# Kernel optimization log

Hardware: AMD Instinct MI355X
Metric: run time of the kernel (lower is better)

The kernel has to match this reference:

```python
import jax, jax.numpy as jnp
import numpy as np

N_NODES = 50000
N_EDGES = 800000
D = 128
SAME_W = 0.3
CROSS_W = 1.0


def setup_inputs() -> dict:
    key = jax.random.key(0)
    k1, k2, k3, k4, k5 = jax.random.split(key, 5)
    x = jax.random.normal(k1, (N_NODES, D), dtype=jnp.float32)
    edge_index = jax.random.randint(k2, (2, N_EDGES), 0, N_NODES, dtype=jnp.int64)
    edge_weight = jax.random.uniform(k3, (N_EDGES,), dtype=jnp.float32)
    Wr1 = jax.random.normal(k4, (D, D), dtype=jnp.float32) * (1.0 / np.sqrt(D))
    Wr2 = jax.random.normal(k5, (D, D), dtype=jnp.float32) * (1.0 / np.sqrt(D))
    return {"x": x, "edge_index": edge_index, "edge_weight": edge_weight,
            "Wr1": Wr1, "Wr2": Wr2, "cell_len": 20000}


def _node_types(idx, cell_len):
    # get_node_types: type 0 if idx <= cell_len, else 1 (note the <=, faithful to source)
    return (idx > cell_len).astype(jnp.int32)


def _conv_layer(x, src, dst, per_edge_w, Wr, n_nodes):
    # gather -> weight -> scatter-mean -> + root linear
    msg = x[src] * per_edge_w[:, None]                       # [E, D]
    agg = jax.ops.segment_sum(msg, dst, num_segments=n_nodes)  # [N, D]
    cnt = jax.ops.segment_sum(jnp.ones_like(per_edge_w), dst, num_segments=n_nodes)
    agg = agg / jnp.maximum(cnt, 1.0)[:, None]               # mean aggr (0 if no edges)
    return agg + x @ Wr.T                                     # lin_r, bias=False


def reference(x, edge_index, edge_weight, Wr1, Wr2, cell_len):
    src, dst = edge_index[0], edge_index[1]
    same = _node_types(src, cell_len) == _node_types(dst, cell_len)
    type_w = jnp.where(same, SAME_W, CROSS_W).astype(x.dtype)
    w = type_w * edge_weight                                  # [E]
    n_nodes = x.shape[0]
    h = _conv_layer(x, src, dst, w, Wr1, n_nodes)
    out = _conv_layer(h, src, dst, w, Wr2, n_nodes)
    return out
```

## Files before the change

kernel.cpp:

```cpp
#include <hip/hip_runtime.h>
#include <cstdint>
#include <cstddef>

#define D 128
#define SAME_W 0.3f
#define CROSS_W 1.0f
#define NSLICE 8
#define CAP 64
#define P1_EPT 8
#define SLAB 131072
#define GEMM_BLOCKS 512

using bf16x8 = __attribute__((ext_vector_type(8))) __bf16;
using f32x4  = __attribute__((ext_vector_type(4))) float;

__device__ __forceinline__ unsigned bf16rne(float f) {
    unsigned u = __float_as_uint(f);
    return (u + 0x7FFFu + ((u >> 16) & 1u)) >> 16;
}

__global__ __launch_bounds__(256) void k_pre(
    const int* __restrict__ src, const int* __restrict__ dst,
    const float* __restrict__ ew, const int* __restrict__ cell_len,
    int* __restrict__ scnt, uint2* __restrict__ ebuf, int E, int sliceLen,
    int nFillC,
    const float4* __restrict__ x4, uint2* __restrict__ xh2,
    uint2* __restrict__ xl2, unsigned* __restrict__ xq, int nvec, int nSplit,
    const float* __restrict__ W1, const float* __restrict__ W2,
    unsigned* __restrict__ wsh, unsigned* __restrict__ w12h,
    unsigned* __restrict__ w12l)
{
    const int b = blockIdx.x;
    if (b < nFillC) {
        __shared__ int lcnt[NSLICE];
        __shared__ int lbase[NSLICE];
        const int t = threadIdx.x;
        if (t < NSLICE) lcnt[t] = 0;
        __syncthreads();
        const int c = *cell_len;
        const int base = b * (256 * P1_EPT) + t;
        int   sl[P1_EPT], rk[P1_EPT];
        uint2 en[P1_EPT];
        #pragma unroll
        for (int u = 0; u < P1_EPT; ++u) {
            int e = base + u * 256;
            sl[u] = -1;
            if (e < E) {
                int d = __builtin_nontemporal_load(&dst[e]);
                int s = __builtin_nontemporal_load(&src[e]);
                float w = __builtin_nontemporal_load(&ew[e]);
                float wt = w * (((s > c) == (d > c)) ? SAME_W : CROSS_W);
                int slice = d / sliceLen;
                sl[u] = slice;
                en[u].x = (unsigned)d | ((unsigned)s << 16);
                en[u].y = bf16rne(wt);
                rk[u] = atomicAdd(&lcnt[slice], 1);
            }
        }
        __syncthreads();
        if (t < NSLICE) lbase[t] = atomicAdd(&scnt[t], lcnt[t]);
        __syncthreads();
        #pragma unroll
        for (int u = 0; u < P1_EPT; ++u) {
            if (sl[u] >= 0) {
                int idx = lbase[sl[u]] + rk[u];
                if (idx < SLAB)
                    ebuf[(size_t)sl[u] * SLAB + idx] = en[u];
            }
        }
    } else if (b < nFillC + nSplit) {
        int i = (b - nFillC) * 256 + threadIdx.x;
        if (i >= nvec) return;
        float4 v = x4[i];
        unsigned h0 = bf16rne(v.x), h1 = bf16rne(v.y),
                 h2 = bf16rne(v.z), h3 = bf16rne(v.w);
        xh2[i] = make_uint2(h0 | (h1 << 16), h2 | (h3 << 16));
        float r0 = v.x - __uint_as_float(h0 << 16);
        float r1 = v.y - __uint_as_float(h1 << 16);
        float r2 = v.z - __uint_as_float(h2 << 16);
        float r3 = v.w - __uint_as_float(h3 << 16);
        xl2[i] = make_uint2(bf16rne(r0) | (bf16rne(r1) << 16),
                            bf16rne(r2) | (bf16rne(r3) << 16));
        int q = __builtin_amdgcn_cvt_pk_fp8_f32(v.x, v.y, 0, false);
        q = __builtin_amdgcn_cvt_pk_fp8_f32(v.z, v.w, q, true);
        xq[i] = (unsigned)q;
    } else {
        int t = (b - nFillC - nSplit) * 256 + threadIdx.x;
        int j = t >> 6, kp = t & 63;
        int k0 = kp * 2;
        float d0 = 0.f, d1 = 0.f;
        #pragma unroll 4
        for (int m = 0; m < D; ++m) {
            float a = W2[j * D + m];
            d0 = fmaf(a, W1[m * D + k0], d0);
            d1 = fmaf(a, W1[m * D + k0 + 1], d1);
        }
        float s0 = W1[j * D + k0] + W2[j * D + k0];
        float s1 = W1[j * D + k0 + 1] + W2[j * D + k0 + 1];
        wsh[j * 64 + kp] = bf16rne(s0) | (bf16rne(s1) << 16);
        unsigned h0 = bf16rne(d0), h1 = bf16rne(d1);
        w12h[j * 64 + kp] = h0 | (h1 << 16);
        float r0 = d0 - __uint_as_float(h0 << 16);
        float r1 = d1 - __uint_as_float(h1 << 16);
        w12l[j * 64 + kp] = bf16rne(r0) | (bf16rne(r1) << 16);
    }
}

__global__ __launch_bounds__(256) void k_scatter(const uint2* __restrict__ ebuf,
                                                 const int* __restrict__ scnt,
                                                 int* __restrict__ cnt,
                                                 unsigned* __restrict__ meta) {
    const int s = blockIdx.x & (NSLICE - 1);
    const int chunk = blockIdx.x >> 3;
    const int n = min(scnt[s], SLAB);
    const uint2* buf = ebuf + (size_t)s * SLAB;
    const int step = (GEMM_BLOCKS / NSLICE) * 256;
    for (int i = chunk * 256 + threadIdx.x; i < n; i += step) {
        uint2 en = buf[i];
        int d = en.x & 0xFFFFu;
        unsigned mw = (en.x >> 16) | (en.y << 16);
        int pos = atomicAdd(&cnt[d], 1);
        if (pos < CAP) meta[d * CAP + pos] = mw;
    }
}

template <bool EMIT_FP8>
__global__ __launch_bounds__(256) void k_agg_fp8(const unsigned short* __restrict__ xq,
                                                 const uint4* __restrict__ meta4,
                                                 const int* __restrict__ cnt,
                                                 unsigned* __restrict__ outb,
                                                 unsigned short* __restrict__ outq,
                                                 int N) {
    int gid = blockIdx.x * blockDim.x + threadIdx.x;
    int node = gid >> 6;
    int lane = gid & 63;
    if (node >= N) return;
    const int cn0 = cnt[node];
    const int cn = min(cn0, CAP);
    const uint4* mrow = meta4 + (size_t)node * (CAP / 4);
    float ax0 = 0.f, ay0 = 0.f, ax1 = 0.f, ay1 = 0.f;
    int i = 0;
    #pragma unroll 1
    for (; i + 16 <= cn; i += 16) {
        uint4 mq[4];
        #pragma unroll
        for (int u = 0; u < 4; ++u) mq[u] = mrow[(i >> 2) + u];
        unsigned short v[16];
        #pragma unroll
        for (int u = 0; u < 16; ++u) {
            unsigned m = ((const unsigned*)mq)[u];
            v[u] = xq[(size_t)(m & 0xFFFFu) * 64 + lane];
        }
        #pragma unroll
        for (int u = 0; u < 16; ++u) {
            unsigned m = ((const unsigned*)mq)[u];
            float wt = __uint_as_float(m & 0xFFFF0000u);
            float vx = __builtin_amdgcn_cvt_f32_fp8((unsigned)v[u], 0);
            float vy = __builtin_amdgcn_cvt_f32_fp8((unsigned)v[u], 1);
            if (u & 1) { ax1 = fmaf(vx, wt, ax1); ay1 = fmaf(vy, wt, ay1); }
            else       { ax0 = fmaf(vx, wt, ax0); ay0 = fmaf(vy, wt, ay0); }
        }
    }
    #pragma unroll 1
    for (; i + 4 <= cn; i += 4) {
        uint4 mq = mrow[i >> 2];
        unsigned short v[4];
        #pragma unroll
        for (int u = 0; u < 4; ++u)
            v[u] = xq[(size_t)(((const unsigned*)&mq)[u] & 0xFFFFu) * 64 + lane];
        #pragma unroll
        for (int u = 0; u < 4; ++u) {
            unsigned m = ((const unsigned*)&mq)[u];
            float wt = __uint_as_float(m & 0xFFFF0000u);
            float vx = __builtin_amdgcn_cvt_f32_fp8((unsigned)v[u], 0);
            float vy = __builtin_amdgcn_cvt_f32_fp8((unsigned)v[u], 1);
            if (u & 1) { ax1 = fmaf(vx, wt, ax1); ay1 = fmaf(vy, wt, ay1); }
            else       { ax0 = fmaf(vx, wt, ax0); ay0 = fmaf(vy, wt, ay0); }
        }
    }
    for (; i < cn; ++i) {
        unsigned m = ((const unsigned*)mrow)[i];
        float wt = __uint_as_float(m & 0xFFFF0000u);
        unsigned short v = xq[(size_t)(m & 0xFFFFu) * 64 + lane];
        ax0 = fmaf(__builtin_amdgcn_cvt_f32_fp8((unsigned)v, 0), wt, ax0);
        ay0 = fmaf(__builtin_amdgcn_cvt_f32_fp8((unsigned)v, 1), wt, ay0);
    }
    const float scale = 1.0f / (float)max(cn0, 1);
    const float rx = (ax0 + ax1) * scale, ry = (ay0 + ay1) * scale;
    outb[(size_t)node * 64 + lane] = bf16rne(rx) | (bf16rne(ry) << 16);
    if (EMIT_FP8) {
        int q = __builtin_amdgcn_cvt_pk_fp8_f32(rx, ry, 0, false);
        outq[(size_t)node * 64 + lane] = (unsigned short)(q & 0xFFFF);
    }
}

__global__ __launch_bounds__(256, 2) void k_gemm2(
    const uint4* __restrict__ xh4, const uint4* __restrict__ xl4,
    const uint4* __restrict__ a1h4,
    const uint4* __restrict__ w12h4, const uint4* __restrict__ w12l4,
    const uint4* __restrict__ wsh4,
    const unsigned* __restrict__ a2b,
    float* __restrict__ fout, int N, int nTiles)
{
    const int t = threadIdx.x;
    const int wave = t >> 6, lane = t & 63;
    const int j0 = wave * 32;
    const int lr = lane & 15;
    const int q  = lane >> 4;

    union FU { uint4 u; bf16x8 v; };

    FU wA[2][4], wB[2][4], wC[2][4];
    #pragma unroll
    for (int jt = 0; jt < 2; ++jt) {
        const int brow = (j0 + jt * 16 + lr) * 16 + q;
        #pragma unroll
        for (int ks = 0; ks < 4; ++ks) {
            wA[jt][ks].u = w12h4[brow + ks * 4];
            wB[jt][ks].u = w12l4[brow + ks * 4];
            wC[jt][ks].u = wsh4[brow + ks * 4];
        }
    }

#define LOAD_TILE(BX, BL, BA, BC, TILE) do {                                   \
    int row_ = (TILE) * 16 + lr; if (row_ > N - 1) row_ = N - 1;               \
    const int ar_ = row_ * 16 + q;                                             \
    _Pragma("unroll")                                                          \
    for (int ks = 0; ks < 4; ++ks) {                                           \
        BX[ks].u = xh4[ar_ + ks * 4];                                          \
        BL[ks].u = xl4[ar_ + ks * 4];                                          \
        BA[ks].u = a1h4[ar_ + ks * 4];                                         \
    }                                                                          \
    _Pragma("unroll")                                                          \
    for (int jt = 0; jt < 2; ++jt)                                             \
        _Pragma("unroll")                                                      \
        for (int r = 0; r < 4; ++r) {                                          \
            int rr_ = (TILE) * 16 + q * 4 + r; if (rr_ > N - 1) rr_ = N - 1;   \
            BC[jt * 4 + r] = a2b[(size_t)rr_ * 64 + ((j0 + jt * 16 + lr) >> 1)]; \
        }                                                                      \
} while (0)

#define COMPUTE_STORE(BX, BL, BA, BC, TILE) do {                               \
    f32x4 c_[2];                                                               \
    c_[0] = (f32x4){0.f, 0.f, 0.f, 0.f};                                       \
    c_[1] = (f32x4){0.f, 0.f, 0.f, 0.f};                                       \
    _Pragma("unroll")                                                          \
    for (int jt = 0; jt < 2; ++jt)                                             \
        _Pragma("unroll")                                                      \
        for (int ks = 0; ks < 4; ++ks) {                                       \
            c_[jt] = __builtin_amdgcn_mfma_f32_16x16x32_bf16(BX[ks].v, wA[jt][ks].v, c_[jt], 0, 0, 0); \
            c_[jt] = __builtin_amdgcn_mfma_f32_16x16x32_bf16(BL[ks].v, wA[jt][ks].v, c_[jt], 0, 0, 0); \
            c_[jt] = __builtin_amdgcn_mfma_f32_16x16x32_bf16(BX[ks].v, wB[jt][ks].v, c_[jt], 0, 0, 0); \
            c_[jt] = __builtin_amdgcn_mfma_f32_16x16x32_bf16(BA[ks].v, wC[jt][ks].v, c_[jt], 0, 0, 0); \
        }                                                                      \
    _Pragma("unroll")                                                          \
    for (int jt = 0; jt < 2; ++jt)                                             \
        _Pragma("unroll")                                                      \
        for (int r = 0; r < 4; ++r) {                                          \
            int rr_ = (TILE) * 16 + q * 4 + r;                                 \
            if (rr_ < N) {                                                     \
                unsigned w_ = BC[jt * 4 + r];                                  \
                float ci_ = __uint_as_float((lr & 1) ? (w_ & 0xFFFF0000u) : (w_ << 16)); \
                fout[(size_t)rr_ * D + j0 + jt * 16 + lr] = c_[jt][r] + ci_;   \
            }                                                                  \
        }                                                                      \
} while (0)

    FU Axh[4], Axl[4], Aa1[4]; unsigned Aci[8];
    FU Bxh[4], Bxl[4], Ba1[4]; unsigned Bci[8];

    int tile = blockIdx.x;
    const int step = gridDim.x;
    if (tile >= nTiles) return;
    LOAD_TILE(Axh, Axl, Aa1, Aci, tile);
    while (true) {
        int tn = tile + step;
        if (tn < nTiles) LOAD_TILE(Bxh, Bxl, Ba1, Bci, tn);
        COMPUTE_STORE(Axh, Axl, Aa1, Aci, tile);
        tile = tn;
        if (tile >= nTiles) break;
        tn = tile + step;
        if (tn < nTiles) LOAD_TILE(Axh, Axl, Aa1, Aci, tn);
        COMPUTE_STORE(Bxh, Bxl, Ba1, Bci, tile);
        tile = tn;
        if (tile >= nTiles) break;
    }
#undef LOAD_TILE
#undef COMPUTE_STORE
}

extern "C" void kernel_launch(void* const* d_in, const int* in_sizes, int n_in,
                              void* d_out, int out_size, void* d_ws, size_t ws_size,
                              hipStream_t stream) {
    const float* x        = (const float*)d_in[0];
    const int*   ei       = (const int*)d_in[1];
    const float* ew       = (const float*)d_in[2];
    const float* Wr1      = (const float*)d_in[3];
    const float* Wr2      = (const float*)d_in[4];
    const int*   cell_len = (const int*)d_in[5];

    const int N = in_sizes[0] / D;
    const int E = in_sizes[1] / 2;
    const int* src = ei;
    const int* dst = ei + E;

    char* ws = (char*)d_ws;
    size_t off = 0;
    unsigned* meta = (unsigned*)(ws + off); off += (size_t)4 * CAP * N;
    int*      cnt  = (int*)     (ws + off); off += (size_t)4 * N;
    int*      scnt = (int*)     (ws + off); off += (size_t)4 * NSLICE;
    off = (off + 255) & ~(size_t)255;
    uint2*    ebuf = (uint2*)   (ws + off); off += (size_t)8 * SLAB * NSLICE;
    unsigned* xh   = (unsigned*)(ws + off); off += (size_t)2 * N * D;
    unsigned* xl   = (unsigned*)(ws + off); off += (size_t)2 * N * D;
    unsigned* a1h  = (unsigned*)(ws + off); off += (size_t)2 * N * D;
    unsigned* a2b  = (unsigned*)(ws + off); off += (size_t)2 * N * D;
    unsigned* xq   = (unsigned*)(ws + off); off += (size_t)1 * N * D;
    unsigned* a1q  = (unsigned*)(ws + off); off += (size_t)1 * N * D;
    unsigned* wsh  = (unsigned*)(ws + off); off += (size_t)2 * D * D;
    unsigned* w12h = (unsigned*)(ws + off); off += (size_t)2 * D * D;
    unsigned* w12l = (unsigned*)(ws + off); off += (size_t)2 * D * D;
    if (ws_size < off) return;
    float* out = (float*)d_out;

    hipMemsetAsync(cnt, 0, (size_t)4 * (N + NSLICE), stream);

    const int sliceLen = (N + NSLICE - 1) / NSLICE;
    const int nFillC = (E + 256 * P1_EPT - 1) / (256 * P1_EPT);
    const int xvec   = N * D / 4;
    const int nSplit = (xvec + 255) / 256;
    const int nW     = (D * 64 + 255) / 256;
    const int aggBlocks = (N + 3) / 4;
    const int nTiles = (N + 15) / 16;

    k_pre<<<nFillC + nSplit + nW, 256, 0, stream>>>(
        src, dst, ew, cell_len, scnt, ebuf, E, sliceLen, nFillC,
        (const float4*)x, (uint2*)xh, (uint2*)xl, xq, xvec, nSplit,
        Wr1, Wr2, wsh, w12h, w12l);

    k_scatter<<<GEMM_BLOCKS, 256, 0, stream>>>(ebuf, scnt, cnt, meta);

    k_agg_fp8<true ><<<aggBlocks, 256, 0, stream>>>(
        (const unsigned short*)xq, (const uint4*)meta, cnt,
        a1h, (unsigned short*)a1q, N);
    k_agg_fp8<false><<<aggBlocks, 256, 0, stream>>>(
        (const unsigned short*)a1q, (const uint4*)meta, cnt,
        a2b, nullptr, N);

    k_gemm2<<<GEMM_BLOCKS, 256, 0, stream>>>((const uint4*)xh, (const uint4*)xl,
                                             (const uint4*)a1h,
                                             (const uint4*)w12h, (const uint4*)w12l,
                                             (const uint4*)wsh, a2b, out, N, nTiles);
}
```

Measured before the change: 227.2 us.

## Fuse second-layer aggregation into GEMM kernel and add nontemporal stores

The second fp8 aggregation pass now runs inside the GEMM kernel. Each wave aggregates four nodes of the 16-row tile into shared memory, then adds the result to the MFMA output, so the a2 intermediate buffer and one kernel launch go away. The scatter grid grows from 512 to 2048 blocks, and streaming writes and reads of ebuf and the x splits use nontemporal hints. In exchange, the GEMM loses its double-buffered tile prefetch and gains two block barriers per tile, so the gather latency now sits serially in front of the MFMA work.

```diff
diff --git a/kernel.cpp b/kernel.cpp
--- a/kernel.cpp
+++ b/kernel.cpp
@@ -10,6 +10,7 @@
 #define P1_EPT 8
 #define SLAB 131072
 #define GEMM_BLOCKS 512
+#define SCAT_BLOCKS 2048
 
 using bf16x8 = __attribute__((ext_vector_type(8))) __bf16;
 using f32x4  = __attribute__((ext_vector_type(4))) float;
@@ -17,6 +18,10 @@
 __device__ __forceinline__ unsigned bf16rne(float f) {
     unsigned u = __float_as_uint(f);
     return (u + 0x7FFFu + ((u >> 16) & 1u)) >> 16;
+}
+__device__ __forceinline__ void nt_store_u2(uint2 v, uint2* p) {
+    unsigned long long val = (unsigned long long)v.x | ((unsigned long long)v.y << 32);
+    __builtin_nontemporal_store(val, (unsigned long long*)p);
 }
 
 __global__ __launch_bounds__(256) void k_pre(
@@ -65,7 +70,7 @@
             if (sl[u] >= 0) {
                 int idx = lbase[sl[u]] + rk[u];
                 if (idx < SLAB)
-                    ebuf[(size_t)sl[u] * SLAB + idx] = en[u];
+                    nt_store_u2(en[u], &ebuf[(size_t)sl[u] * SLAB + idx]);
             }
         }
     } else if (b < nFillC + nSplit) {
@@ -74,16 +79,16 @@
         float4 v = x4[i];
         unsigned h0 = bf16rne(v.x), h1 = bf16rne(v.y),
                  h2 = bf16rne(v.z), h3 = bf16rne(v.w);
-        xh2[i] = make_uint2(h0 | (h1 << 16), h2 | (h3 << 16));
+        nt_store_u2(make_uint2(h0 | (h1 << 16), h2 | (h3 << 16)), &xh2[i]);
         float r0 = v.x - __uint_as_float(h0 << 16);
         float r1 = v.y - __uint_as_float(h1 << 16);
         float r2 = v.z - __uint_as_float(h2 << 16);
         float r3 = v.w - __uint_as_float(h3 << 16);
-        xl2[i] = make_uint2(bf16rne(r0) | (bf16rne(r1) << 16),
-                            bf16rne(r2) | (bf16rne(r3) << 16));
+        nt_store_u2(make_uint2(bf16rne(r0) | (bf16rne(r1) << 16),
+                               bf16rne(r2) | (bf16rne(r3) << 16)), &xl2[i]);
         int q = __builtin_amdgcn_cvt_pk_fp8_f32(v.x, v.y, 0, false);
         q = __builtin_amdgcn_cvt_pk_fp8_f32(v.z, v.w, q, true);
-        xq[i] = (unsigned)q;
+        __builtin_nontemporal_store((unsigned)q, &xq[i]);
     } else {
         int t = (b - nFillC - nSplit) * 256 + threadIdx.x;
         int j = t >> 6, kp = t & 63;
@@ -114,17 +119,18 @@
     const int chunk = blockIdx.x >> 3;
     const int n = min(scnt[s], SLAB);
     const uint2* buf = ebuf + (size_t)s * SLAB;
-    const int step = (GEMM_BLOCKS / NSLICE) * 256;
+    const int step = (SCAT_BLOCKS / NSLICE) * 256;
     for (int i = chunk * 256 + threadIdx.x; i < n; i += step) {
-        uint2 en = buf[i];
-        int d = en.x & 0xFFFFu;
-        unsigned mw = (en.x >> 16) | (en.y << 16);
+        unsigned long long e8 =
+            __builtin_nontemporal_load((const unsigned long long*)&buf[i]);
+        unsigned ex = (unsigned)e8, ey = (unsigned)(e8 >> 32);
+        int d = ex & 0xFFFFu;
+        unsigned mw = (ex >> 16) | (ey << 16);
         int pos = atomicAdd(&cnt[d], 1);
         if (pos < CAP) meta[d * CAP + pos] = mw;
     }
 }
 
-template <bool EMIT_FP8>
 __global__ __launch_bounds__(256) void k_agg_fp8(const unsigned short* __restrict__ xq,
                                                  const uint4* __restrict__ meta4,
                                                  const int* __restrict__ cnt,
@@ -188,20 +194,20 @@
     const float scale = 1.0f / (float)max(cn0, 1);
     const float rx = (ax0 + ax1) * scale, ry = (ay0 + ay1) * scale;
     outb[(size_t)node * 64 + lane] = bf16rne(rx) | (bf16rne(ry) << 16);
-    if (EMIT_FP8) {
-        int q = __builtin_amdgcn_cvt_pk_fp8_f32(rx, ry, 0, false);
-        outq[(size_t)node * 64 + lane] = (unsigned short)(q & 0xFFFF);
-    }
-}
-
-__global__ __launch_bounds__(256, 2) void k_gemm2(
+    int q = __builtin_amdgcn_cvt_pk_fp8_f32(rx, ry, 0, false);
+    outq[(size_t)node * 64 + lane] = (unsigned short)(q & 0xFFFF);
+}
+
+__global__ __launch_bounds__(256, 2) void k_gemm2f(
     const uint4* __restrict__ xh4, const uint4* __restrict__ xl4,
     const uint4* __restrict__ a1h4,
+    const unsigned short* __restrict__ a1q,
+    const uint4* __restrict__ meta4, const int* __restrict__ cnt,
     const uint4* __restrict__ w12h4, const uint4* __restrict__ w12l4,
     const uint4* __restrict__ wsh4,
-    const unsigned* __restrict__ a2b,
     float* __restrict__ fout, int N, int nTiles)
 {
+    __shared__ float a2t[16][132];
     const int t = threadIdx.x;
     const int wave = t >> 6, lane = t & 63;
     const int j0 = wave * 32;
@@ -222,71 +228,101 @@
         }
     }
 
-#define LOAD_TILE(BX, BL, BA, BC, TILE) do {                                   \
-    int row_ = (TILE) * 16 + lr; if (row_ > N - 1) row_ = N - 1;               \
-    const int ar_ = row_ * 16 + q;                                             \
-    _Pragma("unroll")                                                          \
-    for (int ks = 0; ks < 4; ++ks) {                                           \
-        BX[ks].u = xh4[ar_ + ks * 4];                                          \
-        BL[ks].u = xl4[ar_ + ks * 4];                                          \
-        BA[ks].u = a1h4[ar_ + ks * 4];                                         \
-    }                                                                          \
-    _Pragma("unroll")                                                          \
-    for (int jt = 0; jt < 2; ++jt)                                             \
-        _Pragma("unroll")                                                      \
-        for (int r = 0; r < 4; ++r) {                                          \
-            int rr_ = (TILE) * 16 + q * 4 + r; if (rr_ > N - 1) rr_ = N - 1;   \
-            BC[jt * 4 + r] = a2b[(size_t)rr_ * 64 + ((j0 + jt * 16 + lr) >> 1)]; \
-        }                                                                      \
-} while (0)
-
-#define COMPUTE_STORE(BX, BL, BA, BC, TILE) do {                               \
-    f32x4 c_[2];                                                               \
-    c_[0] = (f32x4){0.f, 0.f, 0.f, 0.f};                                       \
-    c_[1] = (f32x4){0.f, 0.f, 0.f, 0.f};                                       \
-    _Pragma("unroll")                                                          \
-    for (int jt = 0; jt < 2; ++jt)                                             \
-        _Pragma("unroll")                                                      \
-        for (int ks = 0; ks < 4; ++ks) {                                       \
-            c_[jt] = __builtin_amdgcn_mfma_f32_16x16x32_bf16(BX[ks].v, wA[jt][ks].v, c_[jt], 0, 0, 0); \
-            c_[jt] = __builtin_amdgcn_mfma_f32_16x16x32_bf16(BL[ks].v, wA[jt][ks].v, c_[jt], 0, 0, 0); \
-            c_[jt] = __builtin_amdgcn_mfma_f32_16x16x32_bf16(BX[ks].v, wB[jt][ks].v, c_[jt], 0, 0, 0); \
-            c_[jt] = __builtin_amdgcn_mfma_f32_16x16x32_bf16(BA[ks].v, wC[jt][ks].v, c_[jt], 0, 0, 0); \
-        }                                                                      \
-    _Pragma("unroll")                                                          \
-    for (int jt = 0; jt < 2; ++jt)                                             \
-        _Pragma("unroll")                                                      \
-        for (int r = 0; r < 4; ++r) {                                          \
-            int rr_ = (TILE) * 16 + q * 4 + r;                                 \
-            if (rr_ < N) {                                                     \
-                unsigned w_ = BC[jt * 4 + r];                                  \
-                float ci_ = __uint_as_float((lr & 1) ? (w_ & 0xFFFF0000u) : (w_ << 16)); \
-                fout[(size_t)rr_ * D + j0 + jt * 16 + lr] = c_[jt][r] + ci_;   \
-            }                                                                  \
-        }                                                                      \
-} while (0)
-
-    FU Axh[4], Axl[4], Aa1[4]; unsigned Aci[8];
-    FU Bxh[4], Bxl[4], Ba1[4]; unsigned Bci[8];
-
-    int tile = blockIdx.x;
-    const int step = gridDim.x;
-    if (tile >= nTiles) return;
-    LOAD_TILE(Axh, Axl, Aa1, Aci, tile);
-    while (true) {
-        int tn = tile + step;
-        if (tn < nTiles) LOAD_TILE(Bxh, Bxl, Ba1, Bci, tn);
-        COMPUTE_STORE(Axh, Axl, Aa1, Aci, tile);
-        tile = tn;
-        if (tile >= nTiles) break;
-        tn = tile + step;
-        if (tn < nTiles) LOAD_TILE(Axh, Axl, Aa1, Aci, tn);
-        COMPUTE_STORE(Bxh, Bxl, Ba1, Bci, tile);
-        tile = tn;
-        if (tile >= nTiles) break;
-    }
-#undef LOAD_TILE
-#undef COMPUTE_STORE
+    for (int tile = blockIdx.x; tile < nTiles; tile += gridDim.x) {
+        FU axh[4], axl[4], aa1[4];
+        {
+            int row = tile * 16 + lr;
+            if (row > N - 1) row = N - 1;
+            const int ar = row * 16 + q;
+            #pragma unroll
+            for (int ks = 0; ks < 4; ++ks) {
+                axh[ks].u = xh4[ar + ks * 4];
+                axl[ks].u = xl4[ar + ks * 4];
+                aa1[ks].u = a1h4[ar + ks * 4];
+            }
+        }
+        #pragma unroll 1
+        for (int nn = 0; nn < 4; ++nn) {
+            const int nl = wave + nn * 4;
+            int node = tile * 16 + nl;
+            if (node > N - 1) node = N - 1;
+            const int cn0 = cnt[node];
+            const int cn = min(cn0, CAP);
+            const uint4* mrow = meta4 + (size_t)node * (CAP / 4);
+            float ax = 0.f, ay = 0.f;
+            int i = 0;
+            #pragma unroll 1
+            for (; i + 16 <= cn; i += 16) {
+                uint4 mq[4];
+                #pragma unroll
+                for (int u = 0; u < 4; ++u) mq[u] = mrow[(i >> 2) + u];
+                unsigned short v[16];
+                #pragma unroll
+                for (int u = 0; u < 16; ++u) {
+                    unsigned m = ((const unsigned*)mq)[u];
+                    v[u] = a1q[(size_t)(m & 0xFFFFu) * 64 + lane];
+                }
+                #pragma unroll
+                for (int u = 0; u < 16; ++u) {
+                    unsigned m = ((const unsigned*)mq)[u];
+                    float wt = __uint_as_float(m & 0xFFFF0000u);
+                    ax = fmaf(__builtin_amdgcn_cvt_f32_fp8((unsigned)v[u], 0), wt, ax);
+                    ay = fmaf(__builtin_amdgcn_cvt_f32_fp8((unsigned)v[u], 1), wt, ay);
+                }
+            }
+            #pragma unroll 1
+            for (; i + 4 <= cn; i += 4) {
+                uint4 mq = mrow[i >> 2];
+                unsigned short v[4];
+                #pragma unroll
+                for (int u = 0; u < 4; ++u)
+                    v[u] = a1q[(size_t)(((const unsigned*)&mq)[u] & 0xFFFFu) * 64 + lane];
+                #pragma unroll
+                for (int u = 0; u < 4; ++u) {
+                    unsigned m = ((const unsigned*)&mq)[u];
+                    float wt = __uint_as_float(m & 0xFFFF0000u);
+                    ax = fmaf(__builtin_amdgcn_cvt_f32_fp8((unsigned)v[u], 0), wt, ax);
+                    ay = fmaf(__builtin_amdgcn_cvt_f32_fp8((unsigned)v[u], 1), wt, ay);
+                }
+            }
+            for (; i < cn; ++i) {
+                unsigned m = ((const unsigned*)mrow)[i];
+                float wt = __uint_as_float(m & 0xFFFF0000u);
+                unsigned short v = a1q[(size_t)(m & 0xFFFFu) * 64 + lane];
+                ax = fmaf(__builtin_amdgcn_cvt_f32_fp8((unsigned)v, 0), wt, ax);
+                ay = fmaf(__builtin_amdgcn_cvt_f32_fp8((unsigned)v, 1), wt, ay);
+            }
+            const float scale = 1.0f / (float)max(cn0, 1);
+            a2t[nl][lane * 2]     = ax * scale;
+            a2t[nl][lane * 2 + 1] = ay * scale;
+        }
+        __syncthreads();
+
+        f32x4 c[2];
+        c[0] = (f32x4){0.f, 0.f, 0.f, 0.f};
+        c[1] = (f32x4){0.f, 0.f, 0.f, 0.f};
+        #pragma unroll
+        for (int jt = 0; jt < 2; ++jt)
+            #pragma unroll
+            for (int ks = 0; ks < 4; ++ks) {
+                c[jt] = __builtin_amdgcn_mfma_f32_16x16x32_bf16(axh[ks].v, wA[jt][ks].v, c[jt], 0, 0, 0);
+                c[jt] = __builtin_amdgcn_mfma_f32_16x16x32_bf16(axl[ks].v, wA[jt][ks].v, c[jt], 0, 0, 0);
+                c[jt] = __builtin_amdgcn_mfma_f32_16x16x32_bf16(axh[ks].v, wB[jt][ks].v, c[jt], 0, 0, 0);
+                c[jt] = __builtin_amdgcn_mfma_f32_16x16x32_bf16(aa1[ks].v, wC[jt][ks].v, c[jt], 0, 0, 0);
+            }
+        #pragma unroll
+        for (int jt = 0; jt < 2; ++jt)
+            #pragma unroll
+            for (int r = 0; r < 4; ++r) {
+                int rr = tile * 16 + q * 4 + r;
+                if (rr < N) {
+                    float res = c[jt][r] + a2t[q * 4 + r][j0 + jt * 16 + lr];
+                    __builtin_nontemporal_store(res,
+                        &fout[(size_t)rr * D + j0 + jt * 16 + lr]);
+                }
+            }
+        __syncthreads();
+    }
 }
 
 extern "C" void kernel_launch(void* const* d_in, const int* in_sizes, int n_in,
@@ -314,7 +350,6 @@
     unsigned* xh   = (unsigned*)(ws + off); off += (size_t)2 * N * D;
     unsigned* xl   = (unsigned*)(ws + off); off += (size_t)2 * N * D;
     unsigned* a1h  = (unsigned*)(ws + off); off += (size_t)2 * N * D;
-    unsigned* a2b  = (unsigned*)(ws + off); off += (size_t)2 * N * D;
     unsigned* xq   = (unsigned*)(ws + off); off += (size_t)1 * N * D;
     unsigned* a1q  = (unsigned*)(ws + off); off += (size_t)1 * N * D;
     unsigned* wsh  = (unsigned*)(ws + off); off += (size_t)2 * D * D;
@@ -338,17 +373,15 @@
         (const float4*)x, (uint2*)xh, (uint2*)xl, xq, xvec, nSplit,
         Wr1, Wr2, wsh, w12h, w12l);
 
-    k_scatter<<<GEMM_BLOCKS, 256, 0, stream>>>(ebuf, scnt, cnt, meta);
-
-    k_agg_fp8<true ><<<aggBlocks, 256, 0, stream>>>(
+    k_scatter<<<SCAT_BLOCKS, 256, 0, stream>>>(ebuf, scnt, cnt, meta);
+
+    k_agg_fp8<<<aggBlocks, 256, 0, stream>>>(
         (const unsigned short*)xq, (const uint4*)meta, cnt,
         a1h, (unsigned short*)a1q, N);
-    k_agg_fp8<false><<<aggBlocks, 256, 0, stream>>>(
+
+    k_gemm2f<<<GEMM_BLOCKS, 256, 0, stream>>>(
+        (const uint4*)xh, (const uint4*)xl, (const uint4*)a1h,
         (const unsigned short*)a1q, (const uint4*)meta, cnt,
-        a2b, nullptr, N);
-
-    k_gemm2<<<GEMM_BLOCKS, 256, 0, stream>>>((const uint4*)xh, (const uint4*)xl,
-                                             (const uint4*)a1h,
-                                             (const uint4*)w12h, (const uint4*)w12l,
-                                             (const uint4*)wsh, a2b, out, N, nTiles);
-}
+        (const uint4*)w12h, (const uint4*)w12l, (const uint4*)wsh,
+        out, N, nTiles);
+}
```

Result: slower. 277.1 us (+22.0%).
